# Kernel optimization log

Hardware: AMD Instinct MI355X
Metric: run time of the kernel (lower is better)

## Reference

```python
import jax, jax.numpy as jnp
import numpy as np

EPS = 1e-5

def _binarize(t):
    # torch Binarize(det) = sign(); .data trick makes autograd see identity (STE)
    return t + jax.lax.stop_gradient(jnp.sign(t) - t)

def _groupnorm1(h, gamma, beta):
    # GroupNorm(num_groups=1): normalize over all channels per sample. h: [B, C]
    mu = jnp.mean(h, axis=1, keepdims=True)
    var = jnp.mean((h - mu) ** 2, axis=1, keepdims=True)
    return (h - mu) * jax.lax.rsqrt(var + EPS) * gamma + beta

def setup_inputs() -> dict:
    key = jax.random.key(0)
    ks = jax.random.split(key, 10)
    B, F, C = 262144, 126, 2
    x = jax.random.normal(ks[0], (B, 1, 1, F), dtype=jnp.float32)
    conv_w = jax.random.normal(ks[1], (F, 1, 1, F), dtype=jnp.float32) * 0.1  # [out_c,in_c,kh,kw]
    gn1_w = jnp.ones((F,), jnp.float32); gn1_b = jnp.zeros((F,), jnp.float32)
    gn2_w = jnp.ones((F,), jnp.float32); gn2_b = jnp.zeros((F,), jnp.float32)
    lin_w = jax.random.normal(ks[2], (C, F), dtype=jnp.float32) * 0.1
    lin_b = jnp.zeros((C,), jnp.float32)
    gn3_w = jnp.ones((C,), jnp.float32); gn3_b = jnp.zeros((C,), jnp.float32)
    return {"x": x, "conv_w": conv_w, "gn1_w": gn1_w, "gn1_b": gn1_b,
            "gn2_w": gn2_w, "gn2_b": gn2_b, "lin_w": lin_w, "lin_b": lin_b,
            "gn3_w": gn3_w, "gn3_b": gn3_b}

def reference(x, conv_w, gn1_w, gn1_b, gn2_w, gn2_b, lin_w, lin_b, gn3_w, gn3_b):
    B = x.shape[0]
    F = conv_w.shape[0]
    # Conv2d(1,126,(1,126)) on [B,1,1,126] collapses to a GEMM over the width axis
    xb = _binarize(x.reshape(B, F))          # [B,126], values in {-1,0,+1}
    wb = _binarize(conv_w.reshape(F, F))     # [126,126]
    h = jnp.einsum('bf,cf->bc', xb, wb)      # conv output, 1x1 spatial squeezed
    h = _groupnorm1(h, gn1_w, gn1_b)         # GroupNorm(1,126) on [B,126,1,1]
    h = jnp.clip(h, -1.0, 1.0)               # Hardtanh
    # Flatten is identity here; second GroupNorm(1,126) + Hardtanh
    h = _groupnorm1(h, gn2_w, gn2_b)
    h = jnp.clip(h, -1.0, 1.0)
    # BNNLinear: binarize input and weight, bias added un-binarized
    hb = _binarize(h)
    lwb = _binarize(lin_w)
    out = jnp.einsum('bf,cf->bc', hb, lwb) + lin_b  # [B,2]
    out = _groupnorm1(out, gn3_w, gn3_b)     # GroupNorm(1,2)
    return out
```

## Files before the change

### kernel.cpp

```cpp
#include <hip/hip_runtime.h>
#include <stdint.h>
#include <math.h>

#define FDIM 126
#define TPB 256
#define BEXT(u, j) ((int)(int8_t)((u) >> ((j) * 8)))

template <typename F>
__device__ __forceinline__ double pw126d(F a) {
    #pragma clang fp contract(off)
    double r0=a(0), r1=a(1), r2=a(2), r3=a(3), r4=a(4), r5=a(5), r6=a(6), r7=a(7);
    for (int i = 8; i < 120; i += 8) {
        r0 += a(i);   r1 += a(i+1); r2 += a(i+2); r3 += a(i+3);
        r4 += a(i+4); r5 += a(i+5); r6 += a(i+6); r7 += a(i+7);
    }
    double res = ((r0 + r1) + (r2 + r3)) + ((r4 + r5) + (r6 + r7));
    res += a(120); res += a(121); res += a(122); res += a(123); res += a(124); res += a(125);
    return res;
}

__global__ __launch_bounds__(TPB) void bnn_v15(
    const float* __restrict__ x,
    const float* __restrict__ conv_w,
    const float* __restrict__ gn1_w, const float* __restrict__ gn1_b,
    const float* __restrict__ gn2_w, const float* __restrict__ gn2_b,
    const float* __restrict__ lin_w, const float* __restrict__ lin_b,
    const float* __restrict__ gn3_w, const float* __restrict__ gn3_b,
    float* __restrict__ out, int nrows)
{
    #pragma clang fp contract(off)
    __shared__ ulonglong2 s_ws[FDIM];
    __shared__ ulonglong2 s_wn[FDIM];
    __shared__ float2 s_g1[FDIM];
    __shared__ float2 s_g2[FDIM];
    __shared__ int8_t s_sl0[128];
    __shared__ int8_t s_sl1[128];
    __shared__ int s_flags;
    __shared__ __align__(16) uint8_t s_pool[TPB * 128];

    ulonglong2* s_xs = (ulonglong2*)s_pool;
    ulonglong2* s_xn = (ulonglong2*)(s_pool + 4096);
    uint32_t*   s_h  = (uint32_t*)s_pool;

    const int t = threadIdx.x;
    const int lane = t & 63;
    const int wv = t >> 6;
    const int64_t row0 = (int64_t)blockIdx.x * TPB;
    const int64_t row = row0 + t;
    const bool rowOK = row < (int64_t)nrows;

    if (t == 0) s_flags = 0;
    __syncthreads();

    for (int r = wv; r < FDIM; r += 4) {
        const float* wr = conv_w + (size_t)r * FDIM;
        float v0 = wr[lane];
        float v1 = (lane < FDIM - 64) ? wr[64 + lane] : 0.f;
        uint64_t ss0 = __ballot(v0 < 0.f);
        uint64_t nn0 = __ballot(v0 != 0.f);
        uint64_t ss1 = __ballot(v1 < 0.f);
        uint64_t nn1 = __ballot(v1 != 0.f);
        if (lane == 0) {
            s_ws[r] = make_ulonglong2(ss0, ss1);
            s_wn[r] = make_ulonglong2(nn0, nn1);
            if (__popcll(nn0) + __popcll(nn1) != FDIM) atomicOr(&s_flags, 1);
        }
    }

    #pragma unroll 4
    for (int k = 0; k < 64; ++k) {
        int lr = (wv << 6) + k;
        int64_t r = row0 + lr;
        bool ok = r < (int64_t)nrows;
        const float* xr = x + r * FDIM;
        float v0 = ok ? xr[lane] : 0.f;
        float v1 = (ok && lane < FDIM - 64) ? xr[64 + lane] : 0.f;
        uint64_t ss0 = __ballot(v0 < 0.f);
        uint64_t nn0 = __ballot(v0 != 0.f);
        uint64_t ss1 = __ballot(v1 < 0.f);
        uint64_t nn1 = __ballot(v1 != 0.f);
        if (lane == 0) {
            s_xs[lr] = make_ulonglong2(ss0, ss1);
            s_xn[lr] = make_ulonglong2(nn0, nn1);
        }
    }

    if (t < FDIM) {
        float g1wv = gn1_w[t], g1bv = gn1_b[t];
        float g2wv = gn2_w[t], g2bv = gn2_b[t];
        s_g1[t] = make_float2(g1wv, g1bv);
        s_g2[t] = make_float2(g2wv, g2bv);
        if (g1wv != 1.f || g1bv != 0.f) atomicOr(&s_flags, 2);
        if (g2wv != 1.f || g2bv != 0.f) atomicOr(&s_flags, 4);
        float l0 = lin_w[t], l1 = lin_w[FDIM + t];
        s_sl0[t] = (int8_t)((l0 > 0.f) - (l0 < 0.f));
        s_sl1[t] = (int8_t)((l1 > 0.f) - (l1 < 0.f));
    }
    __syncthreads();
    const int flags = s_flags;

    const ulonglong2 xs = s_xs[t];
    const ulonglong2 xn = s_xn[t];
    const int Kx = __popcll(xn.x) + __popcll(xn.y);
    __syncthreads();

    int sum = 0;
    if (!(flags & 1)) {
        for (int g = 0; g < 32; ++g) {
            uint32_t pack = 0;
            #pragma unroll
            for (int j = 0; j < 4; ++j) {
                int cc = 4 * g + j;
                if (cc < FDIM) {
                    ulonglong2 w = s_ws[cc];
                    int pc = __popcll((xs.x ^ w.x) & xn.x) + __popcll((xs.y ^ w.y) & xn.y);
                    int h = Kx - 2 * pc;
                    sum += h;
                    pack |= (uint32_t)(h & 255) << (8 * j);
                }
            }
            s_h[g * TPB + t] = pack;
        }
    } else {
        for (int g = 0; g < 32; ++g) {
            uint32_t pack = 0;
            #pragma unroll
            for (int j = 0; j < 4; ++j) {
                int cc = 4 * g + j;
                if (cc < FDIM) {
                    ulonglong2 w = s_ws[cc];
                    ulonglong2 wn = s_wn[cc];
                    uint64_t m0 = xn.x & wn.x, m1 = xn.y & wn.y;
                    int pm = __popcll(m0) + __popcll(m1);
                    int pc = __popcll((xs.x ^ w.x) & m0) + __popcll((xs.y ^ w.y) & m1);
                    int h = pm - 2 * pc;
                    sum += h;
                    pack |= (uint32_t)(h & 255) << (8 * j);
                }
            }
            s_h[g * TPB + t] = pack;
        }
    }

    auto hdw = [&](int g) -> uint32_t { return s_h[g * TPB + t]; };
    auto hget = [&](int i) -> int { return BEXT(hdw(i >> 2), i & 3); };

    const float mu1f = (float)sum / 126.0f;
    float var1f;
    {
        uint32_t u0 = hdw(0), u1 = hdw(1);
        float e;
        e = (float)BEXT(u0,0) - mu1f; float q0 = e*e;
        e = (float)BEXT(u0,1) - mu1f; float q1 = e*e;
        e = (float)BEXT(u0,2) - mu1f; float q2 = e*e;
        e = (float)BEXT(u0,3) - mu1f; float q3 = e*e;
        e = (float)BEXT(u1,0) - mu1f; float q4 = e*e;
        e = (float)BEXT(u1,1) - mu1f; float q5 = e*e;
        e = (float)BEXT(u1,2) - mu1f; float q6 = e*e;
        e = (float)BEXT(u1,3) - mu1f; float q7 = e*e;
        for (int k = 1; k < 15; ++k) {
            uint32_t a0 = hdw(2*k), a1 = hdw(2*k + 1);
            e = (float)BEXT(a0,0) - mu1f; q0 += e*e;
            e = (float)BEXT(a0,1) - mu1f; q1 += e*e;
            e = (float)BEXT(a0,2) - mu1f; q2 += e*e;
            e = (float)BEXT(a0,3) - mu1f; q3 += e*e;
            e = (float)BEXT(a1,0) - mu1f; q4 += e*e;
            e = (float)BEXT(a1,1) - mu1f; q5 += e*e;
            e = (float)BEXT(a1,2) - mu1f; q6 += e*e;
            e = (float)BEXT(a1,3) - mu1f; q7 += e*e;
        }
        float res = ((q0 + q1) + (q2 + q3)) + ((q4 + q5) + (q6 + q7));
        uint32_t u30 = hdw(30), u31 = hdw(31);
        e = (float)BEXT(u30,0) - mu1f; res += e*e;
        e = (float)BEXT(u30,1) - mu1f; res += e*e;
        e = (float)BEXT(u30,2) - mu1f; res += e*e;
        e = (float)BEXT(u30,3) - mu1f; res += e*e;
        e = (float)BEXT(u31,0) - mu1f; res += e*e;
        e = (float)BEXT(u31,1) - mu1f; res += e*e;
        var1f = res / 126.0f;
    }
    const double r1 = 1.0 / sqrt((double)var1f + 1e-5);

    auto c1ofh = [&](int hv) -> double {
        #pragma clang fp contract(off)
        float e32 = (float)hv - mu1f;
        double y = (double)e32 * r1;
        return fmin(fmax(y, -1.0), 1.0);
    };

    int ip0 = 0, ip1 = 0;
    if (!(flags & 6)) {
        double mu2;
        {
            uint32_t u0 = hdw(0), u1 = hdw(1);
            double q0 = c1ofh(BEXT(u0,0)), q1 = c1ofh(BEXT(u0,1));
            double q2 = c1ofh(BEXT(u0,2)), q3 = c1ofh(BEXT(u0,3));
            double q4 = c1ofh(BEXT(u1,0)), q5 = c1ofh(BEXT(u1,1));
            double q6 = c1ofh(BEXT(u1,2)), q7 = c1ofh(BEXT(u1,3));
            for (int k = 1; k < 15; ++k) {
                uint32_t a0 = hdw(2*k), a1 = hdw(2*k + 1);
                q0 += c1ofh(BEXT(a0,0)); q1 += c1ofh(BEXT(a0,1));
                q2 += c1ofh(BEXT(a0,2)); q3 += c1ofh(BEXT(a0,3));
                q4 += c1ofh(BEXT(a1,0)); q5 += c1ofh(BEXT(a1,1));
                q6 += c1ofh(BEXT(a1,2)); q7 += c1ofh(BEXT(a1,3));
            }
            double res = ((q0 + q1) + (q2 + q3)) + ((q4 + q5) + (q6 + q7));
            uint32_t u30 = hdw(30), u31 = hdw(31);
            res += c1ofh(BEXT(u30,0)); res += c1ofh(BEXT(u30,1));
            res += c1ofh(BEXT(u30,2)); res += c1ofh(BEXT(u30,3));
            res += c1ofh(BEXT(u31,0)); res += c1ofh(BEXT(u31,1));
            mu2 = res / 126.0;
        }

        const double c127 = c1ofh(127);
        int lo1 = -127, hi1 = 127, lo2 = -127, hi2 = 127;
        #pragma unroll
        for (int it = 0; it < 8; ++it) {
            int m1 = (lo1 + hi1) >> 1;
            bool ge = (c1ofh(m1) >= mu2);
            hi1 = ge ? m1 : hi1;  lo1 = ge ? lo1 : m1 + 1;
            int m2 = (lo2 + hi2) >> 1;
            bool gt = (c1ofh(m2) > mu2);
            hi2 = gt ? m2 : hi2;  lo2 = gt ? lo2 : m2 + 1;
        }
        const int vge = (c127 >= mu2) ? lo1 : 128;
        const int vgt = (c127 >  mu2) ? lo2 : 128;

        for (int g = 0; g < 31; ++g) {
            uint32_t u = hdw(g);
            #pragma unroll
            for (int j = 0; j < 4; ++j) {
                int c = 4 * g + j;
                int hv = BEXT(u, j);
                int hb = (hv >= vgt) - (hv < vge);
                ip0 += hb * (int)s_sl0[c];
                ip1 += hb * (int)s_sl1[c];
            }
        }
        {
            uint32_t u = hdw(31);
            #pragma unroll
            for (int j = 0; j < 2; ++j) {
                int hv = BEXT(u, j);
                int hb = (hv >= vgt) - (hv < vge);
                ip0 += hb * (int)s_sl0[124 + j];
                ip1 += hb * (int)s_sl1[124 + j];
            }
        }
    } else {
        auto c1f = [&](int i) -> double {
            #pragma clang fp contract(off)
            float e32 = (float)hget(i) - mu1f;
            float2 g = s_g1[i];
            double y = (((double)e32 * r1) * (double)g.x) + (double)g.y;
            return fmin(fmax(y, -1.0), 1.0);
        };
        const double mu2 = pw126d(c1f) / 126.0;
        const double var2 = pw126d([&](int i) -> double {
            #pragma clang fp contract(off)
            double e2 = c1f(i) - mu2;
            return e2 * e2;
        }) / 126.0;
        const double r2 = 1.0 / sqrt(var2 + 1e-5);
        for (int c = 0; c < FDIM; ++c) {
            double e2 = c1f(c) - mu2;
            float2 g2 = s_g2[c];
            double z = ((e2 * r2) * (double)g2.x) + (double)g2.y;
            int hb = (z > 0.0) - (z < 0.0);
            ip0 += hb * (int)s_sl0[c];
            ip1 += hb * (int)s_sl1[c];
        }
    }

    if (rowOK) {
        double o0 = (double)ip0 + (double)lin_b[0];
        double o1 = (double)ip1 + (double)lin_b[1];
        double mu = (o0 + o1) / 2.0;
        double d0 = o0 - mu, d1 = o1 - mu;
        double var = ((d0 * d0) + (d1 * d1)) / 2.0;
        double r3 = 1.0 / sqrt(var + 1e-5);
        double q0 = ((d0 * r3) * (double)gn3_w[0]) + (double)gn3_b[0];
        double q1 = ((d1 * r3) * (double)gn3_w[1]) + (double)gn3_b[1];
        reinterpret_cast<float2*>(out)[row] = make_float2((float)q0, (float)q1);
    }
}

extern "C" void kernel_launch(void* const* d_in, const int* in_sizes, int n_in,
                              void* d_out, int out_size, void* d_ws, size_t ws_size,
                              hipStream_t stream) {
    const float* x      = (const float*)d_in[0];
    const float* conv_w = (const float*)d_in[1];
    const float* gn1_w  = (const float*)d_in[2];
    const float* gn1_b  = (const float*)d_in[3];
    const float* gn2_w  = (const float*)d_in[4];
    const float* gn2_b  = (const float*)d_in[5];
    const float* lin_w  = (const float*)d_in[6];
    const float* lin_b  = (const float*)d_in[7];
    const float* gn3_w  = (const float*)d_in[8];
    const float* gn3_b  = (const float*)d_in[9];

    int nrows = in_sizes[0] / FDIM;
    int nblocks = (nrows + TPB - 1) / TPB;
    bnn_v15<<<nblocks, TPB, 0, stream>>>(x, conv_w, gn1_w, gn1_b, gn2_w, gn2_b,
                                         lin_w, lin_b, gn3_w, gn3_b,
                                         (float*)d_out, nrows);
}
```

Before: 77.52 us.

## Split bit-packing of inputs into a separate kernel before compute

Moves the ballot-based binarization and bit-packing of x and conv_w into a dedicated pack kernel that writes sign/nonzero masks to workspace. The compute kernel then reads its row's packed masks directly from global memory instead of packing them into shared memory in-block. Shared memory drops and the pack stage gets its own launch geometry, which may improve occupancy and overlap. The cost is an extra launch and a round trip through global memory for the packed data. The original fused kernel is kept as a fallback when the workspace is too small.

```diff
diff --git a/kernel.cpp b/kernel.cpp
--- a/kernel.cpp
+++ b/kernel.cpp
@@ -19,9 +19,52 @@
     return res;
 }
 
-__global__ __launch_bounds__(TPB) void bnn_v15(
-    const float* __restrict__ x,
-    const float* __restrict__ conv_w,
+__global__ __launch_bounds__(TPB) void bnn_pack(
+    const float* __restrict__ x, const float* __restrict__ conv_w,
+    ulonglong2* __restrict__ wbuf,
+    ulonglong2* __restrict__ xbuf,
+    int nrows)
+{
+    const int t = threadIdx.x, lane = t & 63, wv = t >> 6;
+    const int64_t row0 = (int64_t)blockIdx.x * 128;
+
+    if (blockIdx.x == 0) {
+        for (int r = wv; r < FDIM; r += 4) {
+            const float* wr = conv_w + (size_t)r * FDIM;
+            float v0 = wr[lane];
+            float v1 = (lane < FDIM - 64) ? wr[64 + lane] : 0.f;
+            uint64_t ss0 = __ballot(v0 < 0.f);
+            uint64_t nn0 = __ballot(v0 != 0.f);
+            uint64_t ss1 = __ballot(v1 < 0.f);
+            uint64_t nn1 = __ballot(v1 != 0.f);
+            if (lane == 0) {
+                wbuf[r]        = make_ulonglong2(ss0, ss1);
+                wbuf[FDIM + r] = make_ulonglong2(nn0, nn1);
+            }
+        }
+    }
+    #pragma unroll 4
+    for (int k = 0; k < 32; ++k) {
+        int lr = (wv << 5) + k;
+        int64_t r = row0 + lr;
+        bool ok = r < (int64_t)nrows;
+        const float* xr = x + r * FDIM;
+        float v0 = ok ? xr[lane] : 0.f;
+        float v1 = (ok && lane < FDIM - 64) ? xr[64 + lane] : 0.f;
+        uint64_t ss0 = __ballot(v0 < 0.f);
+        uint64_t nn0 = __ballot(v0 != 0.f);
+        uint64_t ss1 = __ballot(v1 < 0.f);
+        uint64_t nn1 = __ballot(v1 != 0.f);
+        if (lane == 0 && ok) {
+            xbuf[2 * r]     = make_ulonglong2(ss0, ss1);
+            xbuf[2 * r + 1] = make_ulonglong2(nn0, nn1);
+        }
+    }
+}
+
+__global__ __launch_bounds__(TPB) void bnn_compute(
+    const ulonglong2* __restrict__ wbuf,
+    const ulonglong2* __restrict__ xbuf,
     const float* __restrict__ gn1_w, const float* __restrict__ gn1_b,
     const float* __restrict__ gn2_w, const float* __restrict__ gn2_b,
     const float* __restrict__ lin_w, const float* __restrict__ lin_b,
@@ -36,56 +79,21 @@
     __shared__ int8_t s_sl0[128];
     __shared__ int8_t s_sl1[128];
     __shared__ int s_flags;
-    __shared__ __align__(16) uint8_t s_pool[TPB * 128];
-
-    ulonglong2* s_xs = (ulonglong2*)s_pool;
-    ulonglong2* s_xn = (ulonglong2*)(s_pool + 4096);
-    uint32_t*   s_h  = (uint32_t*)s_pool;
+    __shared__ uint32_t s_h[32 * TPB];
 
     const int t = threadIdx.x;
-    const int lane = t & 63;
-    const int wv = t >> 6;
-    const int64_t row0 = (int64_t)blockIdx.x * TPB;
-    const int64_t row = row0 + t;
+    const int64_t row = (int64_t)blockIdx.x * TPB + t;
     const bool rowOK = row < (int64_t)nrows;
 
     if (t == 0) s_flags = 0;
     __syncthreads();
 
-    for (int r = wv; r < FDIM; r += 4) {
-        const float* wr = conv_w + (size_t)r * FDIM;
-        float v0 = wr[lane];
-        float v1 = (lane < FDIM - 64) ? wr[64 + lane] : 0.f;
-        uint64_t ss0 = __ballot(v0 < 0.f);
-        uint64_t nn0 = __ballot(v0 != 0.f);
-        uint64_t ss1 = __ballot(v1 < 0.f);
-        uint64_t nn1 = __ballot(v1 != 0.f);
-        if (lane == 0) {
-            s_ws[r] = make_ulonglong2(ss0, ss1);
-            s_wn[r] = make_ulonglong2(nn0, nn1);
-            if (__popcll(nn0) + __popcll(nn1) != FDIM) atomicOr(&s_flags, 1);
-        }
-    }
-
-    #pragma unroll 4
-    for (int k = 0; k < 64; ++k) {
-        int lr = (wv << 6) + k;
-        int64_t r = row0 + lr;
-        bool ok = r < (int64_t)nrows;
-        const float* xr = x + r * FDIM;
-        float v0 = ok ? xr[lane] : 0.f;
-        float v1 = (ok && lane < FDIM - 64) ? xr[64 + lane] : 0.f;
-        uint64_t ss0 = __ballot(v0 < 0.f);
-        uint64_t nn0 = __ballot(v0 != 0.f);
-        uint64_t ss1 = __ballot(v1 < 0.f);
-        uint64_t nn1 = __ballot(v1 != 0.f);
-        if (lane == 0) {
-            s_xs[lr] = make_ulonglong2(ss0, ss1);
-            s_xn[lr] = make_ulonglong2(nn0, nn1);
-        }
-    }
-
     if (t < FDIM) {
+        ulonglong2 wsv = wbuf[t];
+        ulonglong2 wnv = wbuf[FDIM + t];
+        s_ws[t] = wsv;
+        s_wn[t] = wnv;
+        if (__popcll(wnv.x) + __popcll(wnv.y) != FDIM) atomicOr(&s_flags, 1);
         float g1wv = gn1_w[t], g1bv = gn1_b[t];
         float g2wv = gn2_w[t], g2bv = gn2_b[t];
         s_g1[t] = make_float2(g1wv, g1bv);
@@ -96,13 +104,15 @@
         s_sl0[t] = (int8_t)((l0 > 0.f) - (l0 < 0.f));
         s_sl1[t] = (int8_t)((l1 > 0.f) - (l1 < 0.f));
     }
+
+    ulonglong2 xs = make_ulonglong2(0, 0), xn = make_ulonglong2(0, 0);
+    if (rowOK) {
+        xs = xbuf[2 * row];
+        xn = xbuf[2 * row + 1];
+    }
+    const int Kx = __popcll(xn.x) + __popcll(xn.y);
     __syncthreads();
     const int flags = s_flags;
-
-    const ulonglong2 xs = s_xs[t];
-    const ulonglong2 xn = s_xn[t];
-    const int Kx = __popcll(xn.x) + __popcll(xn.y);
-    __syncthreads();
 
     int sum = 0;
     if (!(flags & 1)) {
@@ -285,6 +295,269 @@
     }
 }
 
+__global__ __launch_bounds__(TPB) void bnn_v15(
+    const float* __restrict__ x,
+    const float* __restrict__ conv_w,
+    const float* __restrict__ gn1_w, const float* __restrict__ gn1_b,
+    const float* __restrict__ gn2_w, const float* __restrict__ gn2_b,
+    const float* __restrict__ lin_w, const float* __restrict__ lin_b,
+    const float* __restrict__ gn3_w, const float* __restrict__ gn3_b,
+    float* __restrict__ out, int nrows)
+{
+    #pragma clang fp contract(off)
+    __shared__ ulonglong2 s_ws[FDIM];
+    __shared__ ulonglong2 s_wn[FDIM];
+    __shared__ float2 s_g1[FDIM];
+    __shared__ float2 s_g2[FDIM];
+    __shared__ int8_t s_sl0[128];
+    __shared__ int8_t s_sl1[128];
+    __shared__ int s_flags;
+    __shared__ __align__(16) uint8_t s_pool[TPB * 128];
+
+    ulonglong2* s_xs = (ulonglong2*)s_pool;
+    ulonglong2* s_xn = (ulonglong2*)(s_pool + 4096);
+    uint32_t*   s_h  = (uint32_t*)s_pool;
+
+    const int t = threadIdx.x;
+    const int lane = t & 63;
+    const int wv = t >> 6;
+    const int64_t row0 = (int64_t)blockIdx.x * TPB;
+    const int64_t row = row0 + t;
+    const bool rowOK = row < (int64_t)nrows;
+
+    if (t == 0) s_flags = 0;
+    __syncthreads();
+
+    for (int r = wv; r < FDIM; r += 4) {
+        const float* wr = conv_w + (size_t)r * FDIM;
+        float v0 = wr[lane];
+        float v1 = (lane < FDIM - 64) ? wr[64 + lane] : 0.f;
+        uint64_t ss0 = __ballot(v0 < 0.f);
+        uint64_t nn0 = __ballot(v0 != 0.f);
+        uint64_t ss1 = __ballot(v1 < 0.f);
+        uint64_t nn1 = __ballot(v1 != 0.f);
+        if (lane == 0) {
+            s_ws[r] = make_ulonglong2(ss0, ss1);
+            s_wn[r] = make_ulonglong2(nn0, nn1);
+            if (__popcll(nn0) + __popcll(nn1) != FDIM) atomicOr(&s_flags, 1);
+        }
+    }
+    #pragma unroll 4
+    for (int k = 0; k < 64; ++k) {
+        int lr = (wv << 6) + k;
+        int64_t r = row0 + lr;
+        bool ok = r < (int64_t)nrows;
+        const float* xr = x + r * FDIM;
+        float v0 = ok ? xr[lane] : 0.f;
+        float v1 = (ok && lane < FDIM - 64) ? xr[64 + lane] : 0.f;
+        uint64_t ss0 = __ballot(v0 < 0.f);
+        uint64_t nn0 = __ballot(v0 != 0.f);
+        uint64_t ss1 = __ballot(v1 < 0.f);
+        uint64_t nn1 = __ballot(v1 != 0.f);
+        if (lane == 0) {
+            s_xs[lr] = make_ulonglong2(ss0, ss1);
+            s_xn[lr] = make_ulonglong2(nn0, nn1);
+        }
+    }
+    if (t < FDIM) {
+        float g1wv = gn1_w[t], g1bv = gn1_b[t];
+        float g2wv = gn2_w[t], g2bv = gn2_b[t];
+        s_g1[t] = make_float2(g1wv, g1bv);
+        s_g2[t] = make_float2(g2wv, g2bv);
+        if (g1wv != 1.f || g1bv != 0.f) atomicOr(&s_flags, 2);
+        if (g2wv != 1.f || g2bv != 0.f) atomicOr(&s_flags, 4);
+        float l0 = lin_w[t], l1 = lin_w[FDIM + t];
+        s_sl0[t] = (int8_t)((l0 > 0.f) - (l0 < 0.f));
+        s_sl1[t] = (int8_t)((l1 > 0.f) - (l1 < 0.f));
+    }
+    __syncthreads();
+    const int flags = s_flags;
+
+    const ulonglong2 xs = s_xs[t];
+    const ulonglong2 xn = s_xn[t];
+    const int Kx = __popcll(xn.x) + __popcll(xn.y);
+    __syncthreads();
+
+    int sum = 0;
+    if (!(flags & 1)) {
+        for (int g = 0; g < 32; ++g) {
+            uint32_t pack = 0;
+            #pragma unroll
+            for (int j = 0; j < 4; ++j) {
+                int cc = 4 * g + j;
+                if (cc < FDIM) {
+                    ulonglong2 w = s_ws[cc];
+                    int pc = __popcll((xs.x ^ w.x) & xn.x) + __popcll((xs.y ^ w.y) & xn.y);
+                    int h = Kx - 2 * pc;
+                    sum += h;
+                    pack |= (uint32_t)(h & 255) << (8 * j);
+                }
+            }
+            s_h[g * TPB + t] = pack;
+        }
+    } else {
+        for (int g = 0; g < 32; ++g) {
+            uint32_t pack = 0;
+            #pragma unroll
+            for (int j = 0; j < 4; ++j) {
+                int cc = 4 * g + j;
+                if (cc < FDIM) {
+                    ulonglong2 w = s_ws[cc];
+                    ulonglong2 wn = s_wn[cc];
+                    uint64_t m0 = xn.x & wn.x, m1 = xn.y & wn.y;
+                    int pm = __popcll(m0) + __popcll(m1);
+                    int pc = __popcll((xs.x ^ w.x) & m0) + __popcll((xs.y ^ w.y) & m1);
+                    int h = pm - 2 * pc;
+                    sum += h;
+                    pack |= (uint32_t)(h & 255) << (8 * j);
+                }
+            }
+            s_h[g * TPB + t] = pack;
+        }
+    }
+
+    auto hdw = [&](int g) -> uint32_t { return s_h[g * TPB + t]; };
+    auto hget = [&](int i) -> int { return BEXT(hdw(i >> 2), i & 3); };
+
+    const float mu1f = (float)sum / 126.0f;
+    float var1f;
+    {
+        uint32_t u0 = hdw(0), u1 = hdw(1);
+        float e;
+        e = (float)BEXT(u0,0) - mu1f; float q0 = e*e;
+        e = (float)BEXT(u0,1) - mu1f; float q1 = e*e;
+        e = (float)BEXT(u0,2) - mu1f; float q2 = e*e;
+        e = (float)BEXT(u0,3) - mu1f; float q3 = e*e;
+        e = (float)BEXT(u1,0) - mu1f; float q4 = e*e;
+        e = (float)BEXT(u1,1) - mu1f; float q5 = e*e;
+        e = (float)BEXT(u1,2) - mu1f; float q6 = e*e;
+        e = (float)BEXT(u1,3) - mu1f; float q7 = e*e;
+        for (int k = 1; k < 15; ++k) {
+            uint32_t a0 = hdw(2*k), a1 = hdw(2*k + 1);
+            e = (float)BEXT(a0,0) - mu1f; q0 += e*e;
+            e = (float)BEXT(a0,1) - mu1f; q1 += e*e;
+            e = (float)BEXT(a0,2) - mu1f; q2 += e*e;
+            e = (float)BEXT(a0,3) - mu1f; q3 += e*e;
+            e = (float)BEXT(a1,0) - mu1f; q4 += e*e;
+            e = (float)BEXT(a1,1) - mu1f; q5 += e*e;
+            e = (float)BEXT(a1,2) - mu1f; q6 += e*e;
+            e = (float)BEXT(a1,3) - mu1f; q7 += e*e;
+        }
+        float res = ((q0 + q1) + (q2 + q3)) + ((q4 + q5) + (q6 + q7));
+        uint32_t u30 = hdw(30), u31 = hdw(31);
+        e = (float)BEXT(u30,0) - mu1f; res += e*e;
+        e = (float)BEXT(u30,1) - mu1f; res += e*e;
+        e = (float)BEXT(u30,2) - mu1f; res += e*e;
+        e = (float)BEXT(u30,3) - mu1f; res += e*e;
+        e = (float)BEXT(u31,0) - mu1f; res += e*e;
+        e = (float)BEXT(u31,1) - mu1f; res += e*e;
+        var1f = res / 126.0f;
+    }
+    const double r1 = 1.0 / sqrt((double)var1f + 1e-5);
+
+    auto c1ofh = [&](int hv) -> double {
+        #pragma clang fp contract(off)
+        float e32 = (float)hv - mu1f;
+        double y = (double)e32 * r1;
+        return fmin(fmax(y, -1.0), 1.0);
+    };
+
+    int ip0 = 0, ip1 = 0;
+    if (!(flags & 6)) {
+        double mu2;
+        {
+            uint32_t u0 = hdw(0), u1 = hdw(1);
+            double q0 = c1ofh(BEXT(u0,0)), q1 = c1ofh(BEXT(u0,1));
+            double q2 = c1ofh(BEXT(u0,2)), q3 = c1ofh(BEXT(u0,3));
+            double q4 = c1ofh(BEXT(u1,0)), q5 = c1ofh(BEXT(u1,1));
+            double q6 = c1ofh(BEXT(u1,2)), q7 = c1ofh(BEXT(u1,3));
+            for (int k = 1; k < 15; ++k) {
+                uint32_t a0 = hdw(2*k), a1 = hdw(2*k + 1);
+                q0 += c1ofh(BEXT(a0,0)); q1 += c1ofh(BEXT(a0,1));
+                q2 += c1ofh(BEXT(a0,2)); q3 += c1ofh(BEXT(a0,3));
+                q4 += c1ofh(BEXT(a1,0)); q5 += c1ofh(BEXT(a1,1));
+                q6 += c1ofh(BEXT(a1,2)); q7 += c1ofh(BEXT(a1,3));
+            }
+            double res = ((q0 + q1) + (q2 + q3)) + ((q4 + q5) + (q6 + q7));
+            uint32_t u30 = hdw(30), u31 = hdw(31);
+            res += c1ofh(BEXT(u30,0)); res += c1ofh(BEXT(u30,1));
+            res += c1ofh(BEXT(u30,2)); res += c1ofh(BEXT(u30,3));
+            res += c1ofh(BEXT(u31,0)); res += c1ofh(BEXT(u31,1));
+            mu2 = res / 126.0;
+        }
+        const double c127 = c1ofh(127);
+        int lo1 = -127, hi1 = 127, lo2 = -127, hi2 = 127;
+        #pragma unroll
+        for (int it = 0; it < 8; ++it) {
+            int m1 = (lo1 + hi1) >> 1;
+            bool ge = (c1ofh(m1) >= mu2);
+            hi1 = ge ? m1 : hi1;  lo1 = ge ? lo1 : m1 + 1;
+            int m2 = (lo2 + hi2) >> 1;
+            bool gt = (c1ofh(m2) > mu2);
+            hi2 = gt ? m2 : hi2;  lo2 = gt ? lo2 : m2 + 1;
+        }
+        const int vge = (c127 >= mu2) ? lo1 : 128;
+        const int vgt = (c127 >  mu2) ? lo2 : 128;
+
+        for (int g = 0; g < 31; ++g) {
+            uint32_t u = hdw(g);
+            #pragma unroll
+            for (int j = 0; j < 4; ++j) {
+                int c = 4 * g + j;
+                int hv = BEXT(u, j);
+                int hb = (hv >= vgt) - (hv < vge);
+                ip0 += hb * (int)s_sl0[c];
+                ip1 += hb * (int)s_sl1[c];
+            }
+        }
+        {
+            uint32_t u = hdw(31);
+            #pragma unroll
+            for (int j = 0; j < 2; ++j) {
+                int hv = BEXT(u, j);
+                int hb = (hv >= vgt) - (hv < vge);
+                ip0 += hb * (int)s_sl0[124 + j];
+                ip1 += hb * (int)s_sl1[124 + j];
+            }
+        }
+    } else {
+        auto c1f = [&](int i) -> double {
+            #pragma clang fp contract(off)
+            float e32 = (float)hget(i) - mu1f;
+            float2 g = s_g1[i];
+            double y = (((double)e32 * r1) * (double)g.x) + (double)g.y;
+            return fmin(fmax(y, -1.0), 1.0);
+        };
+        const double mu2 = pw126d(c1f) / 126.0;
+        const double var2 = pw126d([&](int i) -> double {
+            #pragma clang fp contract(off)
+            double e2 = c1f(i) - mu2;
+            return e2 * e2;
+        }) / 126.0;
+        const double r2 = 1.0 / sqrt(var2 + 1e-5);
+        for (int c = 0; c < FDIM; ++c) {
+            double e2 = c1f(c) - mu2;
+            float2 g2 = s_g2[c];
+            double z = ((e2 * r2) * (double)g2.x) + (double)g2.y;
+            int hb = (z > 0.0) - (z < 0.0);
+            ip0 += hb * (int)s_sl0[c];
+            ip1 += hb * (int)s_sl1[c];
+        }
+    }
+
+    if (rowOK) {
+        double o0 = (double)ip0 + (double)lin_b[0];
+        double o1 = (double)ip1 + (double)lin_b[1];
+        double mu = (o0 + o1) / 2.0;
+        double d0 = o0 - mu, d1 = o1 - mu;
+        double var = ((d0 * d0) + (d1 * d1)) / 2.0;
+        double r3 = 1.0 / sqrt(var + 1e-5);
+        double q0 = ((d0 * r3) * (double)gn3_w[0]) + (double)gn3_b[0];
+        double q1 = ((d1 * r3) * (double)gn3_w[1]) + (double)gn3_b[1];
+        reinterpret_cast<float2*>(out)[row] = make_float2((float)q0, (float)q1);
+    }
+}
+
 extern "C" void kernel_launch(void* const* d_in, const int* in_sizes, int n_in,
                               void* d_out, int out_size, void* d_ws, size_t ws_size,
                               hipStream_t stream) {
@@ -298,10 +571,22 @@
     const float* lin_b  = (const float*)d_in[7];
     const float* gn3_w  = (const float*)d_in[8];
     const float* gn3_b  = (const float*)d_in[9];
+    float* out = (float*)d_out;
 
     int nrows = in_sizes[0] / FDIM;
-    int nblocks = (nrows + TPB - 1) / TPB;
-    bnn_v15<<<nblocks, TPB, 0, stream>>>(x, conv_w, gn1_w, gn1_b, gn2_w, gn2_b,
-                                         lin_w, lin_b, gn3_w, gn3_b,
-                                         (float*)d_out, nrows);
+    size_t need = 4096 + (size_t)nrows * 32;
+
+    if (d_ws != nullptr && ws_size >= need) {
+        ulonglong2* wbuf = (ulonglong2*)d_ws;
+        ulonglong2* xbuf = (ulonglong2*)((char*)d_ws + 4096);
+        int nb1 = (nrows + 127) / 128;
+        bnn_pack<<<nb1, TPB, 0, stream>>>(x, conv_w, wbuf, xbuf, nrows);
+        int nb2 = (nrows + TPB - 1) / TPB;
+        bnn_compute<<<nb2, TPB, 0, stream>>>(wbuf, xbuf, gn1_w, gn1_b, gn2_w, gn2_b,
+                                             lin_w, lin_b, gn3_w, gn3_b, out, nrows);
+    } else {
+        int nblocks = (nrows + TPB - 1) / TPB;
+        bnn_v15<<<nblocks, TPB, 0, stream>>>(x, conv_w, gn1_w, gn1_b, gn2_w, gn2_b,
+                                             lin_w, lin_b, gn3_w, gn3_b, out, nrows);
+    }
 }
```

Measured after the change: 69.01 us. 1.12x faster.

## Pack conv weights once and split each row across eight lanes

Applied to the files above, without the earlier changes.

Adds a one-block pre-kernel that packs the binarized conv weights into a workspace buffer, so every block no longer rebuilds them from global memory. The main kernel now gives each row 8 lanes, each handling 16 output channels held in registers. GroupNorm reductions use shuffles instead of staging all 126 packed values in shared memory. Each block covers 32 rows instead of 256, which means more blocks and more redundant per-block parameter setup, plus one extra launch. The all-ones weight-mask fast path is dropped, so every channel now takes the masked popcount route.

```diff
diff --git a/kernel.cpp b/kernel.cpp
--- a/kernel.cpp
+++ b/kernel.cpp
@@ -4,6 +4,7 @@
 
 #define FDIM 126
 #define TPB 256
+#define RPB 32
 #define BEXT(u, j) ((int)(int8_t)((u) >> ((j) * 8)))
 
 template <typename F>
@@ -17,6 +18,227 @@
     double res = ((r0 + r1) + (r2 + r3)) + ((r4 + r5) + (r6 + r7));
     res += a(120); res += a(121); res += a(122); res += a(123); res += a(124); res += a(125);
     return res;
+}
+
+__global__ __launch_bounds__(TPB) void bnn_packw(
+    const float* __restrict__ conv_w, ulonglong2* __restrict__ wbuf)
+{
+    const int t = threadIdx.x, lane = t & 63, wv = t >> 6;
+    for (int r = wv; r < FDIM; r += 4) {
+        const float* wr = conv_w + (size_t)r * FDIM;
+        float v0 = wr[lane];
+        float v1 = (lane < FDIM - 64) ? wr[64 + lane] : 0.f;
+        uint64_t ss0 = __ballot(v0 < 0.f);
+        uint64_t nn0 = __ballot(v0 != 0.f);
+        uint64_t ss1 = __ballot(v1 < 0.f);
+        uint64_t nn1 = __ballot(v1 != 0.f);
+        if (lane == 0) {
+            wbuf[r]        = make_ulonglong2(ss0, ss1);
+            wbuf[FDIM + r] = make_ulonglong2(nn0, nn1);
+        }
+    }
+}
+
+__global__ __launch_bounds__(TPB) void bnn_fused(
+    const float* __restrict__ x,
+    const ulonglong2* __restrict__ wbuf,
+    const float* __restrict__ gn1_w, const float* __restrict__ gn1_b,
+    const float* __restrict__ gn2_w, const float* __restrict__ gn2_b,
+    const float* __restrict__ lin_w, const float* __restrict__ lin_b,
+    const float* __restrict__ gn3_w, const float* __restrict__ gn3_b,
+    float* __restrict__ out, int nrows)
+{
+    #pragma clang fp contract(off)
+    __shared__ ulonglong2 s_ws[FDIM];
+    __shared__ ulonglong2 s_wn[FDIM];
+    __shared__ float2 s_g1[FDIM];
+    __shared__ float2 s_g2[FDIM];
+    __shared__ int8_t s_sl0[128];
+    __shared__ int8_t s_sl1[128];
+    __shared__ int s_flags;
+
+    const int t = threadIdx.x;
+    const int lane = t & 63;
+    const int wv = t >> 6;
+    const int grp = lane >> 3;
+    const int j = lane & 7;
+    const int gbase = lane & ~7;
+
+    if (t == 0) s_flags = 0;
+    __syncthreads();
+
+    if (t < 128) { s_sl0[t] = 0; s_sl1[t] = 0; }
+    if (t < FDIM) {
+        s_ws[t] = wbuf[t];
+        s_wn[t] = wbuf[FDIM + t];
+        float g1wv = gn1_w[t], g1bv = gn1_b[t];
+        float g2wv = gn2_w[t], g2bv = gn2_b[t];
+        s_g1[t] = make_float2(g1wv, g1bv);
+        s_g2[t] = make_float2(g2wv, g2bv);
+        if (g1wv != 1.f || g1bv != 0.f) atomicOr(&s_flags, 2);
+        if (g2wv != 1.f || g2bv != 0.f) atomicOr(&s_flags, 4);
+        float l0 = lin_w[t], l1 = lin_w[FDIM + t];
+        s_sl0[t] = (int8_t)((l0 > 0.f) - (l0 < 0.f));
+        s_sl1[t] = (int8_t)((l1 > 0.f) - (l1 < 0.f));
+    }
+    __syncthreads();
+    const int flags = s_flags;
+
+    const int64_t rbase = (int64_t)blockIdx.x * RPB + wv * 8;
+    uint64_t xs0 = 0, xs1 = 0, xn0 = 0, xn1 = 0;
+    #pragma unroll
+    for (int k = 0; k < 8; ++k) {
+        int64_t r = rbase + k;
+        bool ok = r < (int64_t)nrows;
+        const float* xr = x + r * FDIM;
+        float v0 = ok ? xr[lane] : 0.f;
+        float v1 = (ok && lane < FDIM - 64) ? xr[64 + lane] : 0.f;
+        uint64_t ss0 = __ballot(v0 < 0.f);
+        uint64_t nn0 = __ballot(v0 != 0.f);
+        uint64_t ss1 = __ballot(v1 < 0.f);
+        uint64_t nn1 = __ballot(v1 != 0.f);
+        if (k == grp) { xs0 = ss0; xn0 = nn0; xs1 = ss1; xn1 = nn1; }
+    }
+    const int64_t row = rbase + grp;
+    const bool rowOK = row < (int64_t)nrows;
+
+    int hk[16];
+    int sump = 0;
+    #pragma unroll
+    for (int k = 0; k < 16; ++k) {
+        const int c = j + 8 * k;
+        const bool has = (k < 15) || (j < 6);
+        ulonglong2 w  = has ? s_ws[c] : make_ulonglong2(0, 0);
+        ulonglong2 wn = has ? s_wn[c] : make_ulonglong2(0, 0);
+        uint64_t m0 = xn0 & wn.x, m1 = xn1 & wn.y;
+        int pm = __popcll(m0) + __popcll(m1);
+        int pc = __popcll((xs0 ^ w.x) & m0) + __popcll((xs1 ^ w.y) & m1);
+        int hv = has ? (pm - 2 * pc) : 0;
+        hk[k] = hv;
+        sump += hv;
+    }
+    int sum = sump;
+    sum += __shfl_xor(sum, 1); sum += __shfl_xor(sum, 2); sum += __shfl_xor(sum, 4);
+
+    auto treef = [&](float q, float et) -> float {
+        #pragma clang fp contract(off)
+        float v = q + __shfl_xor(q, 1);
+        v = v + __shfl_xor(v, 2);
+        v = v + __shfl_xor(v, 4);
+        #pragma unroll
+        for (int kk = 0; kk < 6; ++kk) v += __shfl(et, gbase + kk, 64);
+        return v;
+    };
+    auto treed = [&](double q, double et) -> double {
+        #pragma clang fp contract(off)
+        double v = q + __shfl_xor(q, 1);
+        v = v + __shfl_xor(v, 2);
+        v = v + __shfl_xor(v, 4);
+        #pragma unroll
+        for (int kk = 0; kk < 6; ++kk) v += __shfl(et, gbase + kk, 64);
+        return v;
+    };
+
+    const float mu1f = (float)sum / 126.0f;
+    float qf, etf = 0.f;
+    {
+        float e = (float)hk[0] - mu1f; qf = e * e;
+        #pragma unroll
+        for (int k = 1; k < 15; ++k) { e = (float)hk[k] - mu1f; qf += e * e; }
+        if (j < 6) { e = (float)hk[15] - mu1f; etf = e * e; }
+    }
+    const float var1f = treef(qf, etf) / 126.0f;
+    const double r1 = 1.0 / sqrt((double)var1f + 1e-5);
+
+    auto c1ofh = [&](int hv) -> double {
+        #pragma clang fp contract(off)
+        float e32 = (float)hv - mu1f;
+        double y = (double)e32 * r1;
+        return fmin(fmax(y, -1.0), 1.0);
+    };
+
+    int ip0 = 0, ip1 = 0;
+    if (!(flags & 6)) {
+        double qd = c1ofh(hk[0]);
+        #pragma unroll
+        for (int k = 1; k < 15; ++k) qd += c1ofh(hk[k]);
+        double etd = (j < 6) ? c1ofh(hk[15]) : 0.0;
+        const double mu2 = treed(qd, etd) / 126.0;
+
+        const double c127 = c1ofh(127);
+        int lo1 = -127, hi1 = 127, lo2 = -127, hi2 = 127;
+        #pragma unroll
+        for (int it = 0; it < 8; ++it) {
+            int m1 = (lo1 + hi1) >> 1;
+            bool ge = (c1ofh(m1) >= mu2);
+            hi1 = ge ? m1 : hi1;  lo1 = ge ? lo1 : m1 + 1;
+            int m2 = (lo2 + hi2) >> 1;
+            bool gt = (c1ofh(m2) > mu2);
+            hi2 = gt ? m2 : hi2;  lo2 = gt ? lo2 : m2 + 1;
+        }
+        const int vge = (c127 >= mu2) ? lo1 : 128;
+        const int vgt = (c127 >  mu2) ? lo2 : 128;
+
+        #pragma unroll
+        for (int k = 0; k < 16; ++k) {
+            const int c = j + 8 * k;
+            const bool has = (k < 15) || (j < 6);
+            int hv = hk[k];
+            int hb = has ? ((hv >= vgt) - (hv < vge)) : 0;
+            ip0 += hb * (int)s_sl0[c & 127];
+            ip1 += hb * (int)s_sl1[c & 127];
+        }
+    } else {
+        auto c1g = [&](int hv, int c) -> double {
+            #pragma clang fp contract(off)
+            float e32 = (float)hv - mu1f;
+            float2 g = s_g1[c];
+            double y = (((double)e32 * r1) * (double)g.x) + (double)g.y;
+            return fmin(fmax(y, -1.0), 1.0);
+        };
+        double qd = c1g(hk[0], j);
+        #pragma unroll
+        for (int k = 1; k < 15; ++k) qd += c1g(hk[k], j + 8 * k);
+        double etd = (j < 6) ? c1g(hk[15], 120 + j) : 0.0;
+        const double mu2 = treed(qd, etd) / 126.0;
+
+        double q2 = 0.0, et2 = 0.0;
+        {
+            double e2 = c1g(hk[0], j) - mu2; q2 = e2 * e2;
+            #pragma unroll
+            for (int k = 1; k < 15; ++k) { double e2b = c1g(hk[k], j + 8 * k) - mu2; q2 += e2b * e2b; }
+            if (j < 6) { double e2b = c1g(hk[15], 120 + j) - mu2; et2 = e2b * e2b; }
+        }
+        const double var2 = treed(q2, et2) / 126.0;
+        const double r2 = 1.0 / sqrt(var2 + 1e-5);
+        #pragma unroll
+        for (int k = 0; k < 16; ++k) {
+            const int c = j + 8 * k;
+            const bool has = (k < 15) || (j < 6);
+            if (has) {
+                double e2 = c1g(hk[k], c) - mu2;
+                float2 g2 = s_g2[c];
+                double z = ((e2 * r2) * (double)g2.x) + (double)g2.y;
+                int hb = (z > 0.0) - (z < 0.0);
+                ip0 += hb * (int)s_sl0[c];
+                ip1 += hb * (int)s_sl1[c];
+            }
+        }
+    }
+    ip0 += __shfl_xor(ip0, 1); ip0 += __shfl_xor(ip0, 2); ip0 += __shfl_xor(ip0, 4);
+    ip1 += __shfl_xor(ip1, 1); ip1 += __shfl_xor(ip1, 2); ip1 += __shfl_xor(ip1, 4);
+
+    if (rowOK && j == 0) {
+        double o0 = (double)ip0 + (double)lin_b[0];
+        double o1 = (double)ip1 + (double)lin_b[1];
+        double mu = (o0 + o1) / 2.0;
+        double d0 = o0 - mu, d1 = o1 - mu;
+        double var = ((d0 * d0) + (d1 * d1)) / 2.0;
+        double r3 = 1.0 / sqrt(var + 1e-5);
+        double q0 = ((d0 * r3) * (double)gn3_w[0]) + (double)gn3_b[0];
+        double q1 = ((d1 * r3) * (double)gn3_w[1]) + (double)gn3_b[1];
+        reinterpret_cast<float2*>(out)[row] = make_float2((float)q0, (float)q1);
+    }
 }
 
 __global__ __launch_bounds__(TPB) void bnn_v15(
@@ -66,7 +288,6 @@
             if (__popcll(nn0) + __popcll(nn1) != FDIM) atomicOr(&s_flags, 1);
         }
     }
-
     #pragma unroll 4
     for (int k = 0; k < 64; ++k) {
         int lr = (wv << 6) + k;
@@ -84,7 +305,6 @@
             s_xn[lr] = make_ulonglong2(nn0, nn1);
         }
     }
-
     if (t < FDIM) {
         float g1wv = gn1_w[t], g1bv = gn1_b[t];
         float g2wv = gn2_w[t], g2bv = gn2_b[t];
@@ -109,14 +329,14 @@
         for (int g = 0; g < 32; ++g) {
             uint32_t pack = 0;
             #pragma unroll
-            for (int j = 0; j < 4; ++j) {
-                int cc = 4 * g + j;
+            for (int jj = 0; jj < 4; ++jj) {
+                int cc = 4 * g + jj;
                 if (cc < FDIM) {
                     ulonglong2 w = s_ws[cc];
                     int pc = __popcll((xs.x ^ w.x) & xn.x) + __popcll((xs.y ^ w.y) & xn.y);
                     int h = Kx - 2 * pc;
                     sum += h;
-                    pack |= (uint32_t)(h & 255) << (8 * j);
+                    pack |= (uint32_t)(h & 255) << (8 * jj);
                 }
             }
             s_h[g * TPB + t] = pack;
@@ -125,8 +345,8 @@
         for (int g = 0; g < 32; ++g) {
             uint32_t pack = 0;
             #pragma unroll
-            for (int j = 0; j < 4; ++j) {
-                int cc = 4 * g + j;
+            for (int jj = 0; jj < 4; ++jj) {
+                int cc = 4 * g + jj;
                 if (cc < FDIM) {
                     ulonglong2 w = s_ws[cc];
                     ulonglong2 wn = s_wn[cc];
@@ -135,7 +355,7 @@
                     int pc = __popcll((xs.x ^ w.x) & m0) + __popcll((xs.y ^ w.y) & m1);
                     int h = pm - 2 * pc;
                     sum += h;
-                    pack |= (uint32_t)(h & 255) << (8 * j);
+                    pack |= (uint32_t)(h & 255) << (8 * jj);
                 }
             }
             s_h[g * TPB + t] = pack;
@@ -211,7 +431,6 @@
             res += c1ofh(BEXT(u31,0)); res += c1ofh(BEXT(u31,1));
             mu2 = res / 126.0;
         }
-
         const double c127 = c1ofh(127);
         int lo1 = -127, hi1 = 127, lo2 = -127, hi2 = 127;
         #pragma unroll
@@ -229,9 +448,9 @@
         for (int g = 0; g < 31; ++g) {
             uint32_t u = hdw(g);
             #pragma unroll
-            for (int j = 0; j < 4; ++j) {
-                int c = 4 * g + j;
-                int hv = BEXT(u, j);
+            for (int jj = 0; jj < 4; ++jj) {
+                int c = 4 * g + jj;
+                int hv = BEXT(u, jj);
                 int hb = (hv >= vgt) - (hv < vge);
                 ip0 += hb * (int)s_sl0[c];
                 ip1 += hb * (int)s_sl1[c];
@@ -240,11 +459,11 @@
         {
             uint32_t u = hdw(31);
             #pragma unroll
-            for (int j = 0; j < 2; ++j) {
-                int hv = BEXT(u, j);
+            for (int jj = 0; jj < 2; ++jj) {
+                int hv = BEXT(u, jj);
                 int hb = (hv >= vgt) - (hv < vge);
-                ip0 += hb * (int)s_sl0[124 + j];
-                ip1 += hb * (int)s_sl1[124 + j];
+                ip0 += hb * (int)s_sl0[124 + jj];
+                ip1 += hb * (int)s_sl1[124 + jj];
             }
         }
     } else {
@@ -298,10 +517,19 @@
     const float* lin_b  = (const float*)d_in[7];
     const float* gn3_w  = (const float*)d_in[8];
     const float* gn3_b  = (const float*)d_in[9];
+    float* out = (float*)d_out;
 
     int nrows = in_sizes[0] / FDIM;
-    int nblocks = (nrows + TPB - 1) / TPB;
-    bnn_v15<<<nblocks, TPB, 0, stream>>>(x, conv_w, gn1_w, gn1_b, gn2_w, gn2_b,
-                                         lin_w, lin_b, gn3_w, gn3_b,
-                                         (float*)d_out, nrows);
+
+    if (d_ws != nullptr && ws_size >= 2 * FDIM * sizeof(ulonglong2)) {
+        ulonglong2* wbuf = (ulonglong2*)d_ws;
+        bnn_packw<<<1, TPB, 0, stream>>>(conv_w, wbuf);
+        int nblocks = (nrows + RPB - 1) / RPB;
+        bnn_fused<<<nblocks, TPB, 0, stream>>>(x, wbuf, gn1_w, gn1_b, gn2_w, gn2_b,
+                                               lin_w, lin_b, gn3_w, gn3_b, out, nrows);
+    } else {
+        int nblocks = (nrows + TPB - 1) / TPB;
+        bnn_v15<<<nblocks, TPB, 0, stream>>>(x, conv_w, gn1_w, gn1_b, gn2_w, gn2_b,
+                                             lin_w, lin_b, gn3_w, gn3_b, out, nrows);
+    }
 }
```

New measurement: 107.6 us. 1.39x slower.
